# Kernel tuning notes

Measured on AMD Instinct MI355X. Metric: run time of the kernel, lower is better.

## Reference

```python
import jax, jax.numpy as jnp
import numpy as np

E, H = 1024, 16


def setup_inputs() -> dict:
    key = jax.random.key(0)
    k1, k2, k3, k4 = jax.random.split(key, 4)
    B, L = 4, 2048
    embeddings = jax.random.normal(k1, (B, L, E), dtype=jnp.float32)
    mask = jax.random.randint(k2, (B, L, L), 0, 2) == 1  # True = masked out
    # Params (torch Linear y = x @ W.T; we store already-transposed [in, out])
    W_qkv = jax.random.normal(k3, (E, 3 * E), dtype=jnp.float32) * 0.02
    W_out = jax.random.normal(k4, (E, E), dtype=jnp.float32) * 0.02
    return {"embeddings": embeddings, "mask": mask, "W_qkv": W_qkv, "W_out": W_out}


def reference(embeddings, mask, W_qkv, W_out):
    B, L, E_ = embeddings.shape
    A = E_ // H
    scale = A ** (-0.5)
    qkv = embeddings @ W_qkv                       # [B, L, 3E]
    qkv = qkv.reshape(B, L, H, 3 * A).transpose(0, 2, 1, 3)  # [B, H, L, 3A]
    q, k, v = jnp.split(qkv, 3, axis=-1)           # each [B, H, L, A]
    scores = jnp.einsum('bhqa,bhka->bhqk', q, k) * scale  # [B, H, L, L]
    m = mask[:, None, :, :]                        # [B, 1, L, L]
    fully = jnp.all(m, axis=-1, keepdims=True)     # rows with every key masked
    scores = jnp.where(m, -jnp.inf, scores)
    scores = jnp.where(fully, 0.0, scores)         # keep softmax finite
    attn = jax.nn.softmax(scores, axis=-1)
    attn = jnp.where(fully, 0.0, attn)             # == torch nan_to_num(0)
    values = jnp.einsum('bhqk,bhka->bhqa', attn, v)  # [B, H, L, A]
    values = values.transpose(0, 2, 1, 3).reshape(B, L, E_)
    return values @ W_out
```

## Files before the change

### kernel.cpp

```cpp
#include <hip/hip_runtime.h>
#include <hip/hip_bf16.h>

#define B_   4
#define L_   2048
#define E_   1024
#define H_   16
#define T_   8192
#define K_   1024

typedef __attribute__((ext_vector_type(8))) short bf16x8;
typedef __attribute__((ext_vector_type(4))) float f32x4;

#define CSC_ (0.125f * 1.44269504f)

__device__ __forceinline__ ushort f2b(float f) {
    union { float f; unsigned u; } x; x.f = f;
    unsigned r = (x.u + 0x7fffu + ((x.u >> 16) & 1u)) >> 16;
    return (ushort)r;
}

__device__ __forceinline__ float fexp2(float x) {
#if __has_builtin(__builtin_amdgcn_exp2f)
    return __builtin_amdgcn_exp2f(x);
#else
    return __expf(x * 0.69314718056f);
#endif
}

__device__ __forceinline__ unsigned pack2bf(float a, float b) {
#if __has_builtin(__builtin_amdgcn_cvt_pk_bf16_f32)
    auto t = __builtin_amdgcn_cvt_pk_bf16_f32(a, b);
    return __builtin_bit_cast(unsigned, t);
#else
    unsigned ua = __builtin_bit_cast(unsigned, a) + 0x8000u;
    unsigned ub = __builtin_bit_cast(unsigned, b) + 0x8000u;
    return __builtin_amdgcn_perm(ub, ua, 0x07060302);
#endif
}

#define GLD_LDS16(gp, lp) __builtin_amdgcn_global_load_lds( \
    (const __attribute__((address_space(1))) void*)(gp), \
    (__attribute__((address_space(3))) void*)(lp), 16, 0, 0)

__global__ void detect_mask_layout(const unsigned char* __restrict__ m, int* flag) {
    __shared__ int s;
    if (threadIdx.x == 0) s = 0;
    __syncthreads();
    int found = 0;
    for (int i = threadIdx.x; i < 4096; i += 256)
        if ((i & 3) != 0 && m[i] != 0) found = 1;
    if (found) atomicOr(&s, 1);
    __syncthreads();
    if (threadIdx.x == 0) *flag = s;
}

__global__ void pack_mask(const void* __restrict__ mraw, const int* __restrict__ flag,
                          unsigned* __restrict__ tbits) {
    int row  = blockIdx.x;
    int lane = threadIdx.x & 63;
    int wave = threadIdx.x >> 6;
    int isByte = *flag;
    int b = row >> 11, q = row & 2047;
    const unsigned char* mb = (const unsigned char*)mraw;
    const int*           mi = (const int*)mraw;
    long long base = (long long)row * L_;
    for (int w = wave; w < 32; w += 4) {
        int idx = w * 64 + lane;
        int v = isByte ? (int)mb[base + idx] : mi[base + idx];
        unsigned long long word = __ballot(v == 0);
        if (lane == 0) {
            tbits[((size_t)b * 64 + 2 * w)     * 2048 + q] = (unsigned)word;
            tbits[((size_t)b * 64 + 2 * w + 1) * 2048 + q] = (unsigned)(word >> 32);
        }
    }
}

__global__ __launch_bounds__(256) void conv_bf16(const float* __restrict__ in,
                                                 ushort* __restrict__ out) {
    int i = blockIdx.x * 256 + threadIdx.x;
    float4 v = ((const float4*)in)[i];
    uint2 o;
    o.x = (unsigned)f2b(v.x) | ((unsigned)f2b(v.y) << 16);
    o.y = (unsigned)f2b(v.z) | ((unsigned)f2b(v.w) << 16);
    ((uint2*)out)[i] = o;
}

__global__ __launch_bounds__(256) void transpose_conv(const float* __restrict__ in,
        ushort* __restrict__ out, int R, int Cn) {
    __shared__ float t[32][33];
    int c0 = blockIdx.x * 32, r0 = blockIdx.y * 32;
    int x = threadIdx.x & 31, y = threadIdx.x >> 5;
#pragma unroll
    for (int k = 0; k < 4; ++k)
        t[y + k * 8][x] = in[(size_t)(r0 + y + k * 8) * Cn + c0 + x];
    __syncthreads();
#pragma unroll
    for (int k = 0; k < 4; ++k)
        out[(size_t)(c0 + y + k * 8) * R + r0 + x] = f2b(t[x][y + k * 8]);
}

template<int NDIM, int MODE>
__global__ __launch_bounds__(256) void gemm_bf16(
        const ushort* __restrict__ Ab, const ushort* __restrict__ Bt,
        float* __restrict__ Cg, ushort* __restrict__ Qb,
        ushort* __restrict__ Kb, ushort* __restrict__ Vt) {
    __shared__ ushort As[128 * 64];
    __shared__ ushort Bs[128 * 64];
    const int tid = threadIdx.x;
    const int wv = tid >> 6, ln = tid & 63;
    const int bn = blockIdx.x * 128, bm = blockIdx.y * 128;
    const int wm = (wv & 1) * 64, wn = (wv >> 1) * 64;
    const int row16 = ln & 15, quad = ln >> 4;
    const int cg8 = (((ln & 7) ^ (ln >> 3)) * 8);

    f32x4 acc[4][4];
#pragma unroll
    for (int i = 0; i < 4; ++i)
#pragma unroll
        for (int j = 0; j < 4; ++j) acc[i][j] = (f32x4){0.f, 0.f, 0.f, 0.f};

    for (int k0 = 0; k0 < K_; k0 += 64) {
        __syncthreads();
#pragma unroll
        for (int it = 0; it < 4; ++it) {
            int rA = wv * 32 + it * 8 + (ln >> 3);
            GLD_LDS16(Ab + (size_t)(bm + rA) * K_ + k0 + cg8, &As[(wv * 32 + it * 8) * 64]);
            GLD_LDS16(Bt + (size_t)(bn + rA) * K_ + k0 + cg8, &Bs[(wv * 32 + it * 8) * 64]);
        }
        __syncthreads();
#pragma unroll
        for (int ks = 0; ks < 2; ++ks) {
            const int ch = (((ks * 4 + quad) ^ (ln & 7)) * 8);
            bf16x8 af[4], bf[4];
#pragma unroll
            for (int i = 0; i < 4; ++i)
                af[i] = *(const bf16x8*)&As[(wm + i * 16 + row16) * 64 + ch];
#pragma unroll
            for (int j = 0; j < 4; ++j)
                bf[j] = *(const bf16x8*)&Bs[(wn + j * 16 + row16) * 64 + ch];
#pragma unroll
            for (int i = 0; i < 4; ++i)
#pragma unroll
                for (int j = 0; j < 4; ++j)
                    acc[i][j] = __builtin_amdgcn_mfma_f32_16x16x32_bf16(
                        af[i], bf[j], acc[i][j], 0, 0, 0);
        }
    }

    if (MODE == 0) {
#pragma unroll
        for (int i = 0; i < 4; ++i)
#pragma unroll
            for (int j = 0; j < 4; ++j) {
                int col = bn + wn + j * 16 + row16;
#pragma unroll
                for (int r = 0; r < 4; ++r) {
                    int row = bm + wm + i * 16 + quad * 4 + r;
                    Cg[(size_t)row * NDIM + col] = acc[i][j][r];
                }
            }
    } else {
#pragma unroll
        for (int j = 0; j < 4; ++j) {
            int col = bn + wn + j * 16 + row16;
            int h = col / 192, w = col - h * 192;
            int sel = w >> 6, a = w & 63;
            float qs = (sel == 0) ? CSC_ : 1.0f;
#pragma unroll
            for (int i = 0; i < 4; ++i)
#pragma unroll
                for (int r = 0; r < 4; ++r) {
                    int rowg = bm + wm + i * 16 + quad * 4 + r;
                    int b = rowg >> 11, l = rowg & 2047;
                    ushort v = f2b(acc[i][j][r] * qs);
                    size_t bh = (size_t)(b * H_ + h);
                    if (sel == 0)      Qb[(bh * L_ + l) * 64 + a] = v;
                    else if (sel == 1) Kb[(bh * L_ + l) * 64 + a] = v;
                    else {
                        int k5 = l & 31;
                        int lp = (l & ~31) | (2 * (k5 & 15) + (k5 >> 4));
                        Vt[(bh * 64 + a) * L_ + lp] = v;
                    }
                }
        }
    }
}

__global__ __launch_bounds__(256) void attn_mfma(
        const ushort* __restrict__ Qb, const ushort* __restrict__ Kb,
        const ushort* __restrict__ Vt, const unsigned* __restrict__ tbits,
        ushort* __restrict__ vals) {
    __shared__ ushort KV[6][2048];
    __shared__ ushort Ps[4][1280];

    const int tid = threadIdx.x, wv = tid >> 6, ln = tid & 63;
    const int bh = blockIdx.y, b = bh >> 4, h = bh & 15;
    const int q0 = blockIdx.x * 128;
    const int row16 = ln & 15, quad = ln >> 4;
    const int lh = ln >> 3, ll = ln & 7;
    const int cg8 = ((ll ^ lh) * 8);

    const ushort* Kg = Kb + (size_t)bh * L_ * 64;
    const ushort* Vg = Vt + (size_t)bh * 64 * L_;

    const int vc4 = ll ^ lh;
    const ushort* vsrc = Vg + (size_t)(wv * 8 + lh + 32 * (vc4 >> 2)) * L_ + (vc4 & 3) * 8;
    const ushort* ksrc = Kg + (size_t)(wv * 8 + lh) * 64 + cg8;

    {
        const ushort* Qgw = Qb + ((size_t)bh * L_ + q0 + wv * 32) * 64;
#pragma unroll
        for (int it = 0; it < 4; ++it)
            GLD_LDS16(Qgw + (size_t)(it * 8 + lh) * 64 + cg8, &KV[wv][it * 8 * 64]);
    }
    __syncthreads();
    bf16x8 aq[2][2];
#pragma unroll
    for (int rg = 0; rg < 2; ++rg)
#pragma unroll
        for (int ks = 0; ks < 2; ++ks)
            aq[rg][ks] = *(const bf16x8*)&KV[wv][(rg * 16 + row16) * 64 +
                                                 (((ks * 4 + quad) ^ (row16 & 7)) * 8)];
    __syncthreads();

    GLD_LDS16(ksrc,        &KV[0][(wv * 8) * 64]);
    GLD_LDS16(ksrc + 2048, &KV[1][(wv * 8) * 64]);
    GLD_LDS16(vsrc,        &KV[3][(wv * 8) * 64]);
    GLD_LDS16(vsrc + 32,   &KV[4][(wv * 8) * 64]);

    ushort *kc = KV[0], *kn = KV[1], *kf = KV[2];
    ushort *vcb = KV[3], *vnb = KV[4], *vfb = KV[5];
    const ushort* kstage = ksrc + 2 * 2048;
    const ushort* vstage = vsrc + 2 * 32;

    ushort* Pw = Ps[wv];
    bf16x8 vone;
#pragma unroll
    for (int i = 0; i < 8; ++i) vone[i] = (short)0x3F80;

    f32x4 oacc[2][4], lacc[2];
#pragma unroll
    for (int rg = 0; rg < 2; ++rg) {
        lacc[rg] = (f32x4){0.f, 0.f, 0.f, 0.f};
#pragma unroll
        for (int t = 0; t < 4; ++t) oacc[rg][t] = (f32x4){0.f, 0.f, 0.f, 0.f};
    }

    const unsigned* mptr = tbits + (size_t)b * 64 * 2048 + (q0 + wv * 32 + quad * 4);

    auto qk = [&](const ushort* kbuf, f32x4 (&s)[2][2]) {
#pragma unroll
        for (int rg = 0; rg < 2; ++rg)
#pragma unroll
            for (int t = 0; t < 2; ++t) s[rg][t] = (f32x4){0.f, 0.f, 0.f, 0.f};
#pragma unroll
        for (int ks = 0; ks < 2; ++ks) {
            bf16x8 bk[2];
#pragma unroll
            for (int t = 0; t < 2; ++t)
                bk[t] = *(const bf16x8*)&kbuf[(t * 16 + row16) * 64 +
                                              (((ks * 4 + quad) ^ (row16 & 7)) * 8)];
#pragma unroll
            for (int rg = 0; rg < 2; ++rg)
#pragma unroll
                for (int t = 0; t < 2; ++t)
                    s[rg][t] = __builtin_amdgcn_mfma_f32_16x16x32_bf16(
                        aq[rg][ks], bk[t], s[rg][t], 0, 0, 0);
        }
    };

    auto softmax_pv = [&](f32x4 (&sa)[2][2], uint4 m0, uint4 m1) {
#pragma unroll
        for (int rg = 0; rg < 2; ++rg) {
            const unsigned* wr = rg ? (const unsigned*)&m1 : (const unsigned*)&m0;
#pragma unroll
            for (int r = 0; r < 4; ++r) {
                unsigned sh = wr[r] >> row16;
                unsigned pk = pack2bf(fexp2(sa[rg][0][r]), fexp2(sa[rg][1][r]));
                pk &= (sh & 0x00010001u) * 0xFFFFu;
                *(unsigned*)&Pw[(rg * 16 + quad * 4 + r) * 40 + 2 * row16] = pk;
            }
        }
        bf16x8 bv[4];
#pragma unroll
        for (int t = 0; t < 4; ++t)
            bv[t] = *(const bf16x8*)&vcb[((t & 1) * 16 + row16) * 64 +
                                         ((((t >> 1) * 4 + quad) ^ (row16 & 7)) * 8)];
#pragma unroll
        for (int rg = 0; rg < 2; ++rg) {
            bf16x8 ap = *(const bf16x8*)&Pw[(rg * 16 + row16) * 40 + quad * 8];
            lacc[rg] = __builtin_amdgcn_mfma_f32_16x16x32_bf16(ap, vone, lacc[rg], 0, 0, 0);
#pragma unroll
            for (int t = 0; t < 4; ++t)
                oacc[rg][t] = __builtin_amdgcn_mfma_f32_16x16x32_bf16(
                    ap, bv[t], oacc[rg][t], 0, 0, 0);
        }
    };

    auto body = [&](bool do_stage, f32x4 (&sa)[2][2], f32x4 (&sn)[2][2],
                    uint4 (&mc)[2], uint4 (&mn)[2]) {
        mn[0] = *(const uint4*)(mptr);
        mn[1] = *(const uint4*)(mptr + 16);
        mptr += 2048;
        if (do_stage) {
            GLD_LDS16(kstage, &kf[(wv * 8) * 64]);
            GLD_LDS16(vstage, &vfb[(wv * 8) * 64]);
            kstage += 2048; vstage += 32;
        }
        qk(kn, sn);
        softmax_pv(sa, mc[0], mc[1]);
        __syncthreads();
        ushort* t;
        t = kc;  kc  = kn;  kn  = kf;  kf  = t;
        t = vcb; vcb = vnb; vnb = vfb; vfb = t;
    };

    uint4 mA[2], mB[2];
    mA[0] = *(const uint4*)(mptr);
    mA[1] = *(const uint4*)(mptr + 16);
    mptr += 2048;
    f32x4 sA[2][2], sB[2][2];
    __syncthreads();
    qk(kc, sA);

    for (int i = 0; i < 31; ++i) {
        body(true, sA, sB, mA, mB);
        body(2 * i + 1 < 62, sB, sA, mB, mA);
    }
    body(false, sA, sB, mA, mB);
    softmax_pv(sB, mB[0], mB[1]);

#pragma unroll
    for (int rg = 0; rg < 2; ++rg)
#pragma unroll
        for (int r = 0; r < 4; ++r) {
            float l = lacc[rg][r];
            float inv = (l > 0.f) ? 1.0f / l : 0.f;
            int qrow = q0 + wv * 32 + rg * 16 + quad * 4 + r;
            size_t base = ((size_t)b * L_ + qrow) * E_ + h * 64;
#pragma unroll
            for (int t = 0; t < 4; ++t)
                vals[base + t * 16 + row16] = f2b(oacc[rg][t][r] * inv);
        }
}

extern "C" void kernel_launch(void* const* d_in, const int* in_sizes, int n_in,
                              void* d_out, int out_size, void* d_ws, size_t ws_size,
                              hipStream_t stream) {
    const float* emb  = (const float*)d_in[0];
    const void*  mask = d_in[1];
    const float* wqkv = (const float*)d_in[2];
    const float* wout = (const float*)d_in[3];
    float* out = (float*)d_out;

    char* ws = (char*)d_ws;
    const size_t NEED = 4096ull + 2097152ull + 2ull * 46137344ull;
    if (ws_size < NEED) return;

    int* flag = (int*)ws;
    unsigned* tbits = (unsigned*)(ws + 4096);
    ushort* embb  = (ushort*)(ws + 4096 + 2097152);
    ushort* Wqkvt = embb  + 8388608;
    ushort* Wott  = Wqkvt + 3145728;
    ushort* Qb    = Wott  + 1048576;
    ushort* Kb    = Qb    + 8388608;
    ushort* Vt    = Kb    + 8388608;
    ushort* vals  = Vt    + 8388608;

    detect_mask_layout<<<1, 256, 0, stream>>>((const unsigned char*)mask, flag);
    pack_mask<<<T_, 256, 0, stream>>>(mask, flag, tbits);
    conv_bf16<<<8192, 256, 0, stream>>>(emb, embb);
    transpose_conv<<<dim3(96, 32), 256, 0, stream>>>(wqkv, Wqkvt, 1024, 3072);
    transpose_conv<<<dim3(32, 32), 256, 0, stream>>>(wout, Wott, 1024, 1024);
    gemm_bf16<3072, 1><<<dim3(24, 64), 256, 0, stream>>>(
        embb, Wqkvt, nullptr, Qb, Kb, Vt);
    attn_mfma<<<dim3(16, 64), 256, 0, stream>>>(Qb, Kb, Vt, tbits, vals);
    gemm_bf16<1024, 0><<<dim3(8, 64), 256, 0, stream>>>(
        vals, Wott, out, nullptr, nullptr, nullptr);
}
```

Baseline: 387.8 us.

## Split attention block into 8 waves of 16 query rows with split K/V staging

The attention kernel moves from 4 waves each owning 32 query rows to 8 waves each owning 16 rows, with a 512-thread block and launch bounds asking for 4 blocks per CU. K tiles are now staged by waves 0-3 and V tiles by waves 4-7, so each wave issues one async load per step instead of two. MFMA sections are wrapped in s_setprio so matrix work is favoured when waves interleave. The aim is more waves per CU to hide latency and lower register pressure per wave. The cost is twice as many K/V LDS reads per query row, since each K/V tile is now shared across 8 waves instead of 4, and barrier sync spans more waves.

```diff
diff --git a/kernel.cpp b/kernel.cpp
--- a/kernel.cpp
+++ b/kernel.cpp
@@ -186,12 +186,12 @@
     }
 }
 
-__global__ __launch_bounds__(256) void attn_mfma(
+__global__ __launch_bounds__(512, 4) void attn_mfma(
         const ushort* __restrict__ Qb, const ushort* __restrict__ Kb,
         const ushort* __restrict__ Vt, const unsigned* __restrict__ tbits,
         ushort* __restrict__ vals) {
     __shared__ ushort KV[6][2048];
-    __shared__ ushort Ps[4][1280];
+    __shared__ ushort Ps[8][640];
 
     const int tid = threadIdx.x, wv = tid >> 6, ln = tid & 63;
     const int bh = blockIdx.y, b = bh >> 4, h = bh & 15;
@@ -203,30 +203,32 @@
     const ushort* Kg = Kb + (size_t)bh * L_ * 64;
     const ushort* Vg = Vt + (size_t)bh * 64 * L_;
 
+    const int wk = wv & 3;
+    const bool isK = (wv < 4);
     const int vc4 = ll ^ lh;
-    const ushort* vsrc = Vg + (size_t)(wv * 8 + lh + 32 * (vc4 >> 2)) * L_ + (vc4 & 3) * 8;
-    const ushort* ksrc = Kg + (size_t)(wv * 8 + lh) * 64 + cg8;
+    const ushort* vsrc = Vg + (size_t)(wk * 8 + lh + 32 * (vc4 >> 2)) * L_ + (vc4 & 3) * 8;
+    const ushort* ksrc = Kg + (size_t)(wk * 8 + lh) * 64 + cg8;
 
     {
-        const ushort* Qgw = Qb + ((size_t)bh * L_ + q0 + wv * 32) * 64;
-#pragma unroll
-        for (int it = 0; it < 4; ++it)
-            GLD_LDS16(Qgw + (size_t)(it * 8 + lh) * 64 + cg8, &KV[wv][it * 8 * 64]);
-    }
-    __syncthreads();
-    bf16x8 aq[2][2];
-#pragma unroll
-    for (int rg = 0; rg < 2; ++rg)
-#pragma unroll
-        for (int ks = 0; ks < 2; ++ks)
-            aq[rg][ks] = *(const bf16x8*)&KV[wv][(rg * 16 + row16) * 64 +
-                                                 (((ks * 4 + quad) ^ (row16 & 7)) * 8)];
-    __syncthreads();
-
-    GLD_LDS16(ksrc,        &KV[0][(wv * 8) * 64]);
-    GLD_LDS16(ksrc + 2048, &KV[1][(wv * 8) * 64]);
-    GLD_LDS16(vsrc,        &KV[3][(wv * 8) * 64]);
-    GLD_LDS16(vsrc + 32,   &KV[4][(wv * 8) * 64]);
+        const ushort* Qgw = Qb + ((size_t)bh * L_ + q0 + wv * 16) * 64;
+        GLD_LDS16(Qgw + (size_t)lh * 64 + cg8,       &KV[0][(wv * 16) * 64]);
+        GLD_LDS16(Qgw + (size_t)(8 + lh) * 64 + cg8, &KV[0][(wv * 16 + 8) * 64]);
+    }
+    __syncthreads();
+    bf16x8 aq[2];
+#pragma unroll
+    for (int ks = 0; ks < 2; ++ks)
+        aq[ks] = *(const bf16x8*)&KV[0][(wv * 16 + row16) * 64 +
+                                        (((ks * 4 + quad) ^ (row16 & 7)) * 8)];
+    __syncthreads();
+
+    if (isK) {
+        GLD_LDS16(ksrc,        &KV[0][(wk * 8) * 64]);
+        GLD_LDS16(ksrc + 2048, &KV[1][(wk * 8) * 64]);
+    } else {
+        GLD_LDS16(vsrc,        &KV[3][(wk * 8) * 64]);
+        GLD_LDS16(vsrc + 32,   &KV[4][(wk * 8) * 64]);
+    }
 
     ushort *kc = KV[0], *kn = KV[1], *kf = KV[2];
     ushort *vcb = KV[3], *vnb = KV[4], *vfb = KV[5];
@@ -238,21 +240,16 @@
 #pragma unroll
     for (int i = 0; i < 8; ++i) vone[i] = (short)0x3F80;
 
-    f32x4 oacc[2][4], lacc[2];
-#pragma unroll
-    for (int rg = 0; rg < 2; ++rg) {
-        lacc[rg] = (f32x4){0.f, 0.f, 0.f, 0.f};
-#pragma unroll
-        for (int t = 0; t < 4; ++t) oacc[rg][t] = (f32x4){0.f, 0.f, 0.f, 0.f};
-    }
-
-    const unsigned* mptr = tbits + (size_t)b * 64 * 2048 + (q0 + wv * 32 + quad * 4);
-
-    auto qk = [&](const ushort* kbuf, f32x4 (&s)[2][2]) {
-#pragma unroll
-        for (int rg = 0; rg < 2; ++rg)
-#pragma unroll
-            for (int t = 0; t < 2; ++t) s[rg][t] = (f32x4){0.f, 0.f, 0.f, 0.f};
+    f32x4 oacc[4], lacc = (f32x4){0.f, 0.f, 0.f, 0.f};
+#pragma unroll
+    for (int t = 0; t < 4; ++t) oacc[t] = (f32x4){0.f, 0.f, 0.f, 0.f};
+
+    const unsigned* mptr = tbits + (size_t)b * 64 * 2048 + (q0 + wv * 16 + quad * 4);
+
+    auto qk = [&](const ushort* kbuf, f32x4 (&s)[2]) {
+#pragma unroll
+        for (int t = 0; t < 2; ++t) s[t] = (f32x4){0.f, 0.f, 0.f, 0.f};
+        __builtin_amdgcn_s_setprio(1);
 #pragma unroll
         for (int ks = 0; ks < 2; ++ks) {
             bf16x8 bk[2];
@@ -261,65 +258,57 @@
                 bk[t] = *(const bf16x8*)&kbuf[(t * 16 + row16) * 64 +
                                               (((ks * 4 + quad) ^ (row16 & 7)) * 8)];
 #pragma unroll
-            for (int rg = 0; rg < 2; ++rg)
-#pragma unroll
-                for (int t = 0; t < 2; ++t)
-                    s[rg][t] = __builtin_amdgcn_mfma_f32_16x16x32_bf16(
-                        aq[rg][ks], bk[t], s[rg][t], 0, 0, 0);
-        }
+            for (int t = 0; t < 2; ++t)
+                s[t] = __builtin_amdgcn_mfma_f32_16x16x32_bf16(
+                    aq[ks], bk[t], s[t], 0, 0, 0);
+        }
+        __builtin_amdgcn_s_setprio(0);
     };
 
-    auto softmax_pv = [&](f32x4 (&sa)[2][2], uint4 m0, uint4 m1) {
-#pragma unroll
-        for (int rg = 0; rg < 2; ++rg) {
-            const unsigned* wr = rg ? (const unsigned*)&m1 : (const unsigned*)&m0;
-#pragma unroll
-            for (int r = 0; r < 4; ++r) {
-                unsigned sh = wr[r] >> row16;
-                unsigned pk = pack2bf(fexp2(sa[rg][0][r]), fexp2(sa[rg][1][r]));
-                pk &= (sh & 0x00010001u) * 0xFFFFu;
-                *(unsigned*)&Pw[(rg * 16 + quad * 4 + r) * 40 + 2 * row16] = pk;
-            }
+    auto softmax_pv = [&](f32x4 (&sa)[2], uint4 m) {
+        const unsigned* wr = (const unsigned*)&m;
+#pragma unroll
+        for (int r = 0; r < 4; ++r) {
+            unsigned sh = wr[r] >> row16;
+            unsigned pk = pack2bf(fexp2(sa[0][r]), fexp2(sa[1][r]));
+            pk &= (sh & 0x00010001u) * 0xFFFFu;
+            *(unsigned*)&Pw[(quad * 4 + r) * 40 + 2 * row16] = pk;
         }
         bf16x8 bv[4];
 #pragma unroll
         for (int t = 0; t < 4; ++t)
             bv[t] = *(const bf16x8*)&vcb[((t & 1) * 16 + row16) * 64 +
                                          ((((t >> 1) * 4 + quad) ^ (row16 & 7)) * 8)];
-#pragma unroll
-        for (int rg = 0; rg < 2; ++rg) {
-            bf16x8 ap = *(const bf16x8*)&Pw[(rg * 16 + row16) * 40 + quad * 8];
-            lacc[rg] = __builtin_amdgcn_mfma_f32_16x16x32_bf16(ap, vone, lacc[rg], 0, 0, 0);
-#pragma unroll
-            for (int t = 0; t < 4; ++t)
-                oacc[rg][t] = __builtin_amdgcn_mfma_f32_16x16x32_bf16(
-                    ap, bv[t], oacc[rg][t], 0, 0, 0);
-        }
+        bf16x8 ap = *(const bf16x8*)&Pw[row16 * 40 + quad * 8];
+        __builtin_amdgcn_s_setprio(1);
+        lacc = __builtin_amdgcn_mfma_f32_16x16x32_bf16(ap, vone, lacc, 0, 0, 0);
+#pragma unroll
+        for (int t = 0; t < 4; ++t)
+            oacc[t] = __builtin_amdgcn_mfma_f32_16x16x32_bf16(
+                ap, bv[t], oacc[t], 0, 0, 0);
+        __builtin_amdgcn_s_setprio(0);
     };
 
-    auto body = [&](bool do_stage, f32x4 (&sa)[2][2], f32x4 (&sn)[2][2],
-                    uint4 (&mc)[2], uint4 (&mn)[2]) {
-        mn[0] = *(const uint4*)(mptr);
-        mn[1] = *(const uint4*)(mptr + 16);
+    auto body = [&](bool do_stage, f32x4 (&sa)[2], f32x4 (&sn)[2],
+                    uint4 &mc, uint4 &mn) {
+        mn = *(const uint4*)(mptr);
         mptr += 2048;
         if (do_stage) {
-            GLD_LDS16(kstage, &kf[(wv * 8) * 64]);
-            GLD_LDS16(vstage, &vfb[(wv * 8) * 64]);
-            kstage += 2048; vstage += 32;
+            if (isK) { GLD_LDS16(kstage, &kf[(wk * 8) * 64]);  kstage += 2048; }
+            else     { GLD_LDS16(vstage, &vfb[(wk * 8) * 64]); vstage += 32; }
         }
         qk(kn, sn);
-        softmax_pv(sa, mc[0], mc[1]);
+        softmax_pv(sa, mc);
         __syncthreads();
         ushort* t;
         t = kc;  kc  = kn;  kn  = kf;  kf  = t;
         t = vcb; vcb = vnb; vnb = vfb; vfb = t;
     };
 
-    uint4 mA[2], mB[2];
-    mA[0] = *(const uint4*)(mptr);
-    mA[1] = *(const uint4*)(mptr + 16);
+    uint4 mA, mB;
+    mA = *(const uint4*)(mptr);
     mptr += 2048;
-    f32x4 sA[2][2], sB[2][2];
+    f32x4 sA[2], sB[2];
     __syncthreads();
     qk(kc, sA);
 
@@ -328,20 +317,18 @@
         body(2 * i + 1 < 62, sB, sA, mB, mA);
     }
     body(false, sA, sB, mA, mB);
-    softmax_pv(sB, mB[0], mB[1]);
-
-#pragma unroll
-    for (int rg = 0; rg < 2; ++rg)
-#pragma unroll
-        for (int r = 0; r < 4; ++r) {
-            float l = lacc[rg][r];
-            float inv = (l > 0.f) ? 1.0f / l : 0.f;
-            int qrow = q0 + wv * 32 + rg * 16 + quad * 4 + r;
-            size_t base = ((size_t)b * L_ + qrow) * E_ + h * 64;
-#pragma unroll
-            for (int t = 0; t < 4; ++t)
-                vals[base + t * 16 + row16] = f2b(oacc[rg][t][r] * inv);
-        }
+    softmax_pv(sB, mB);
+
+#pragma unroll
+    for (int r = 0; r < 4; ++r) {
+        float l = lacc[r];
+        float inv = (l > 0.f) ? 1.0f / l : 0.f;
+        int qrow = q0 + wv * 16 + quad * 4 + r;
+        size_t base = ((size_t)b * L_ + qrow) * E_ + h * 64;
+#pragma unroll
+        for (int t = 0; t < 4; ++t)
+            vals[base + t * 16 + row16] = f2b(oacc[t][r] * inv);
+    }
 }
 
 extern "C" void kernel_launch(void* const* d_in, const int* in_sizes, int n_in,
@@ -374,7 +361,7 @@
     transpose_conv<<<dim3(32, 32), 256, 0, stream>>>(wout, Wott, 1024, 1024);
     gemm_bf16<3072, 1><<<dim3(24, 64), 256, 0, stream>>>(
         embb, Wqkvt, nullptr, Qb, Kb, Vt);
-    attn_mfma<<<dim3(16, 64), 256, 0, stream>>>(Qb, Kb, Vt, tbits, vals);
+    attn_mfma<<<dim3(16, 64), 512, 0, stream>>>(Qb, Kb, Vt, tbits, vals);
     gemm_bf16<1024, 0><<<dim3(8, 64), 256, 0, stream>>>(
         vals, Wott, out, nullptr, nullptr, nullptr);
 }
```

Result: faster. 372.1 us (-4.0%).
